# Kernel tuning notes

Measured on AMD Instinct MI355X. Metric: run time of the kernel, lower is better.

Reference implementation:

```python
import jax, jax.numpy as jnp
import numpy as np

TOP_K = 2


def setup_inputs() -> dict:
    key = jax.random.key(0)
    k1, k2 = jax.random.split(key)
    x = jax.random.normal(k1, (4, 4096, 2048), dtype=jnp.float32)
    W = jax.random.normal(k2, (64, 2048), dtype=jnp.float32) * (1.0 / np.sqrt(2048))
    return {"x": x, "W": W}


def reference(x, W):
    B, S, D = x.shape
    E = W.shape[0]
    # logits: [B*S, E] via linear router (no bias)
    flat = x.reshape(-1, D)
    logits = jnp.einsum('td,ed->te', flat, W)
    probs = jax.nn.softmax(logits, axis=-1)
    # eval path: top-k indices
    _, top_k_indices = jax.lax.top_k(probs, TOP_K)          # [T, K]
    # scatter 1s -> mask; scatter gathered probs -> router_probs (== probs*mask)
    router_mask = jax.nn.one_hot(top_k_indices, E, dtype=probs.dtype).sum(axis=-2)  # [T, E]
    router_probs = probs * router_mask
    # normalize (top_k > 1: gradient flows through the sum)
    router_probs = router_probs / router_probs.sum(axis=-1, keepdims=True)
    return (router_mask.reshape(B, S, E),
            top_k_indices.reshape(B, S, TOP_K),
            router_probs.reshape(B, S, E),
            probs.reshape(B, S, E))
```

## Files before the change

### kernel.cpp

```cpp
#include <hip/hip_runtime.h>
#include <math.h>


#define D_DIM 2048
#define E_DIM 64

typedef __bf16 bf16x8 __attribute__((ext_vector_type(8)));
typedef unsigned short us8 __attribute__((ext_vector_type(8)));
typedef float f32x4 __attribute__((ext_vector_type(4)));

static __device__ __forceinline__ unsigned short f2bf(float f) {
    unsigned int u = __float_as_uint(f);
    u += 0x7fffu + ((u >> 16) & 1u);
    return (unsigned short)(u >> 16);
}
static __device__ __forceinline__ float bf2f(unsigned short h) {
    return __uint_as_float(((unsigned int)h) << 16);
}
static __device__ __forceinline__ void split4(const float4 v, ushort4* h, ushort4* l) {
    h->x = f2bf(v.x); l->x = f2bf(v.x - bf2f(h->x));
    h->y = f2bf(v.y); l->y = f2bf(v.y - bf2f(h->y));
    h->z = f2bf(v.z); l->z = f2bf(v.z - bf2f(h->z));
    h->w = f2bf(v.w); l->w = f2bf(v.w - bf2f(h->w));
}

static __device__ __forceinline__ void gld_lds16(const void* g, void* l) {
    __builtin_amdgcn_global_load_lds(
        (const __attribute__((address_space(1))) unsigned int*)g,
        (__attribute__((address_space(3))) unsigned int*)l,
        16, 0, 0);
}

__global__ __launch_bounds__(256, 1) void convert_w(
    const float4* __restrict__ W4, unsigned short* __restrict__ WH,
    unsigned short* __restrict__ WL)
{
    int i = blockIdx.x * 256 + threadIdx.x;
    float4 v = W4[i];
    ushort4 h, l;
    split4(v, &h, &l);
    *(ushort4*)&WH[i * 4] = h;
    *(ushort4*)&WL[i * 4] = l;
}

template<int KS>
__global__ __launch_bounds__(256, 3) void gemm_part(
    const float* __restrict__ x,
    const unsigned short* __restrict__ WHg, const unsigned short* __restrict__ WLg,
    float* __restrict__ P, int T)
{
    __shared__ __align__(16) float XF[2][64 * 64];

    const int tid  = threadIdx.x;
    const int lane = tid & 63;
    const int wv   = tid >> 6;
    const int quad = lane >> 4;
    const int l16  = lane & 15;

    const int ntb = T >> 6;
    const int tb  = blockIdx.x % ntb;
    const int ksl = blockIdx.x / ntb;
    const int t0  = tb << 6;
    const int NCH = (D_DIM / KS) >> 6;
    const int k0  = ksl * (D_DIM / KS);

    f32x4 acc[4];
    #pragma unroll
    for (int n = 0; n < 4; ++n) { f32x4 z = {0.f, 0.f, 0.f, 0.f}; acc[n] = z; }

    const int srow = wv * 4 + (lane >> 4);
    const int scg  = lane & 15;

    #pragma unroll
    for (int i = 0; i < 4; ++i) {
        int row = i * 16 + srow;
        int cg  = scg ^ (row & 15);
        gld_lds16(x + (size_t)(t0 + row) * D_DIM + k0 + cg * 4,
                  &XF[0][(i * 256 + wv * 64) * 4]);
    }

    for (int ch = 0; ch < NCH; ++ch) {
        const int buf = ch & 1;
        const int kc  = k0 + (ch << 6);

        bf16x8 bh[2][4], bl[2][4];
        #pragma unroll
        for (int ks2 = 0; ks2 < 2; ++ks2)
            #pragma unroll
            for (int n = 0; n < 4; ++n) {
                const size_t wo = (size_t)(n * 16 + l16) * D_DIM + kc + ks2 * 32 + quad * 8;
                bh[ks2][n] = *(const bf16x8*)(WHg + wo);
                bl[ks2][n] = *(const bf16x8*)(WLg + wo);
            }

        {
            const int chn = (ch + 1) & (NCH - 1);
            const int kcn = k0 + (chn << 6);
            #pragma unroll
            for (int i = 0; i < 4; ++i) {
                int row = i * 16 + srow;
                int cg  = scg ^ (row & 15);
                gld_lds16(x + (size_t)(t0 + row) * D_DIM + kcn + cg * 4,
                          &XF[buf ^ 1][(i * 256 + wv * 64) * 4]);
            }
        }

        asm volatile("s_waitcnt vmcnt(20)" ::: "memory");
        __builtin_amdgcn_s_barrier();

        #pragma unroll
        for (int ks2 = 0; ks2 < 2; ++ks2) {
            const int tr = wv * 16 + l16;
            const int c0 = ks2 * 8 + quad * 2;
            float4 xa = *(const float4*)&XF[buf][(tr * 16 + ( c0      ^ (tr & 15))) * 4];
            float4 xb = *(const float4*)&XF[buf][(tr * 16 + ((c0 + 1) ^ (tr & 15))) * 4];
            ushort4 h0, l0, h1, l1;
            split4(xa, &h0, &l0);
            split4(xb, &h1, &l1);
            union { us8 u; bf16x8 b; } ua, ul;
            ua.u = (us8){h0.x, h0.y, h0.z, h0.w, h1.x, h1.y, h1.z, h1.w};
            ul.u = (us8){l0.x, l0.y, l0.z, l0.w, l1.x, l1.y, l1.z, l1.w};

            #pragma unroll
            for (int n = 0; n < 4; ++n) {
                acc[n] = __builtin_amdgcn_mfma_f32_16x16x32_bf16(ua.b, bh[ks2][n], acc[n], 0, 0, 0);
                acc[n] = __builtin_amdgcn_mfma_f32_16x16x32_bf16(ul.b, bh[ks2][n], acc[n], 0, 0, 0);
                acc[n] = __builtin_amdgcn_mfma_f32_16x16x32_bf16(ua.b, bl[ks2][n], acc[n], 0, 0, 0);
            }
        }

        __builtin_amdgcn_s_barrier();
    }

    float* Pb = P + ((size_t)ksl * T + t0) * 64;
    #pragma unroll
    for (int n = 0; n < 4; ++n)
        #pragma unroll
        for (int r = 0; r < 4; ++r)
            Pb[(wv * 16 + quad * 4 + r) * 64 + n * 16 + l16] = acc[n][r];
}

template<int KS>
__global__ __launch_bounds__(256, 4) void reduce_router(
    const float* __restrict__ P, int T,
    float* __restrict__ mask_out, float* __restrict__ idx_out,
    float* __restrict__ rp_out, float* __restrict__ probs_out)
{
    const int tid  = threadIdx.x;
    const int lane = tid & 63;
    const int wv   = tid >> 6;

    for (int i = 0; i < 4; ++i) {
        int t = blockIdx.x * 16 + wv * 4 + i;
        float v = 0.f;
        #pragma unroll
        for (int s = 0; s < KS; ++s)
            v += P[((size_t)s * T + t) * 64 + lane];

        float bv = v; int bi = lane;
        #pragma unroll
        for (int off = 1; off < 64; off <<= 1) {
            float ov = __shfl_xor(bv, off, 64);
            int   oi = __shfl_xor(bi, off, 64);
            bool take = (ov > bv) || (ov == bv && oi < bi);
            bv = take ? ov : bv;
            bi = take ? oi : bi;
        }
        float m = bv; int i1 = bi;

        float p = __expf(v - m);
        float s = p;
        #pragma unroll
        for (int off = 1; off < 64; off <<= 1) s += __shfl_xor(s, off, 64);
        float prob = p / s;

        float v2 = (lane == i1) ? -INFINITY : v;
        float bv2 = v2; int bi2 = lane;
        #pragma unroll
        for (int off = 1; off < 64; off <<= 1) {
            float ov = __shfl_xor(bv2, off, 64);
            int   oi = __shfl_xor(bi2, off, 64);
            bool take = (ov > bv2) || (ov == bv2 && oi < bi2);
            bv2 = take ? ov : bv2;
            bi2 = take ? oi : bi2;
        }
        int i2 = bi2;

        float pd = __shfl(prob, i1, 64) + __shfl(prob, i2, 64);
        bool top = (lane == i1) || (lane == i2);

        mask_out[(size_t)t * 64 + lane]  = top ? 1.f : 0.f;
        rp_out[(size_t)t * 64 + lane]    = top ? prob / pd : 0.f;
        probs_out[(size_t)t * 64 + lane] = prob;
        if (lane == 0) {
            idx_out[(size_t)t * 2]     = (float)i1;
            idx_out[(size_t)t * 2 + 1] = (float)i2;
        }
    }
}

extern "C" void kernel_launch(void* const* d_in, const int* in_sizes, int n_in,
                              void* d_out, int out_size, void* d_ws, size_t ws_size,
                              hipStream_t stream) {
    const float* x = (const float*)d_in[0];
    const float* W = (const float*)d_in[1];
    float* out = (float*)d_out;

    const int T  = in_sizes[0] / D_DIM;
    const int WN = in_sizes[1];

    unsigned short* WH = (unsigned short*)d_ws;
    unsigned short* WL = WH + WN;
    float* P = (float*)(WL + WN);

    float* mask_out  = out;
    float* idx_out   = out + (size_t)T * E_DIM;
    float* rp_out    = idx_out + (size_t)T * 2;
    float* probs_out = rp_out + (size_t)T * E_DIM;

    const size_t avail = ws_size - (size_t)WN * 4;
    const size_t slice_bytes = (size_t)T * 64 * 4;

    convert_w<<<dim3(WN / 1024), dim3(256), 0, stream>>>((const float4*)W, WH, WL);

    if (avail >= 4 * slice_bytes) {
        gemm_part<4><<<dim3((T / 64) * 4), dim3(256), 0, stream>>>(x, WH, WL, P, T);
        reduce_router<4><<<dim3(T / 16), dim3(256), 0, stream>>>(
            P, T, mask_out, idx_out, rp_out, probs_out);
    } else if (avail >= 2 * slice_bytes) {
        gemm_part<2><<<dim3((T / 64) * 2), dim3(256), 0, stream>>>(x, WH, WL, P, T);
        reduce_router<2><<<dim3(T / 16), dim3(256), 0, stream>>>(
            P, T, mask_out, idx_out, rp_out, probs_out);
    } else {
        gemm_part<1><<<dim3(T / 64), dim3(256), 0, stream>>>(x, WH, WL, P, T);
        reduce_router<1><<<dim3(T / 16), dim3(256), 0, stream>>>(
            P, T, mask_out, idx_out, rp_out, probs_out);
    }
}
```

Measured before the change: 229.0 us.

## Restructure router GEMM into single-wave blocks with 4-stage LDS ring and pre-swizzled W

Replaces the 256-thread, 64-token GEMM blocks with 64-thread single-wave blocks over 32 tokens. They use a 4-deep LDS ring of x tiles loaded asynchronously three steps ahead, with no block barriers. W is pre-packed into an MFMA-fragment-ordered hi/lo bf16 layout so each lane does one contiguous 16-byte load per fragment, and the next step's W fragments are register double-buffered. The split-K factor is fixed at 4 and the workspace-size fallbacks are dropped. This aims to hide memory latency with finer-grained waves and deeper prefetch, at the cost of more blocks and redundant W traffic per token.

```diff
diff --git a/kernel.cpp b/kernel.cpp
--- a/kernel.cpp
+++ b/kernel.cpp
@@ -4,10 +4,14 @@
 
 #define D_DIM 2048
 #define E_DIM 64
+#define KS 4
+#define KSTEPS 16
 
 typedef __bf16 bf16x8 __attribute__((ext_vector_type(8)));
 typedef unsigned short us8 __attribute__((ext_vector_type(8)));
 typedef float f32x4 __attribute__((ext_vector_type(4)));
+
+#define FENCE asm volatile("" ::: "memory")
 
 static __device__ __forceinline__ unsigned short f2bf(float f) {
     unsigned int u = __float_as_uint(f);
@@ -32,115 +36,126 @@
 }
 
 __global__ __launch_bounds__(256, 1) void convert_w(
-    const float4* __restrict__ W4, unsigned short* __restrict__ WH,
-    unsigned short* __restrict__ WL)
+    const float* __restrict__ W, unsigned short* __restrict__ WB)
 {
-    int i = blockIdx.x * 256 + threadIdx.x;
-    float4 v = W4[i];
-    ushort4 h, l;
-    split4(v, &h, &l);
-    *(ushort4*)&WH[i * 4] = h;
-    *(ushort4*)&WL[i * 4] = l;
-}
-
-template<int KS>
-__global__ __launch_bounds__(256, 3) void gemm_part(
-    const float* __restrict__ x,
-    const unsigned short* __restrict__ WHg, const unsigned short* __restrict__ WLg,
+    int u = blockIdx.x * 256 + threadIdx.x;
+    int lane = u & 63;
+    int r = u >> 6;
+    int h = r & 1;  r >>= 1;
+    int n = r & 3;  int sg = r >> 2;
+    int E  = n * 16 + (lane & 15);
+    int k0 = sg * 32 + (lane >> 4) * 8;
+    const float4* src = (const float4*)(W + (size_t)E * D_DIM + k0);
+    float4 a = src[0], b = src[1];
+    ushort4 ha, la, hb, lb;
+    split4(a, &ha, &la);
+    split4(b, &hb, &lb);
+    us8 out = h ? (us8){la.x, la.y, la.z, la.w, lb.x, lb.y, lb.z, lb.w}
+                : (us8){ha.x, ha.y, ha.z, ha.w, hb.x, hb.y, hb.z, hb.w};
+    *(us8*)(WB + (size_t)u * 8) = out;
+}
+
+__global__ __launch_bounds__(64, 2) void gemm_part(
+    const float* __restrict__ x, const unsigned short* __restrict__ WB,
     float* __restrict__ P, int T)
 {
-    __shared__ __align__(16) float XF[2][64 * 64];
-
-    const int tid  = threadIdx.x;
-    const int lane = tid & 63;
-    const int wv   = tid >> 6;
+    __shared__ __align__(16) float RING[4][1024];
+
+    const int lane = threadIdx.x;
     const int quad = lane >> 4;
     const int l16  = lane & 15;
 
-    const int ntb = T >> 6;
+    const int ntb = T >> 5;
     const int tb  = blockIdx.x % ntb;
     const int ksl = blockIdx.x / ntb;
-    const int t0  = tb << 6;
-    const int NCH = (D_DIM / KS) >> 6;
-    const int k0  = ksl * (D_DIM / KS);
-
-    f32x4 acc[4];
+    const int t0  = tb << 5;
+    const int kb  = ksl * (D_DIM / KS);
+
+    const int srow = lane >> 2;
+    const int scg  = (lane & 3) ^ ((lane >> 3) & 3);
+
+    f32x4 acc[2][4];
     #pragma unroll
-    for (int n = 0; n < 4; ++n) { f32x4 z = {0.f, 0.f, 0.f, 0.f}; acc[n] = z; }
-
-    const int srow = wv * 4 + (lane >> 4);
-    const int scg  = lane & 15;
+    for (int g = 0; g < 2; ++g)
+        #pragma unroll
+        for (int n = 0; n < 4; ++n) { f32x4 z = {0.f, 0.f, 0.f, 0.f}; acc[g][n] = z; }
+
+    auto stage = [&](int s) {
+        const int kc = kb + s * 32;
+        #pragma unroll
+        for (int j = 0; j < 4; ++j) {
+            int g = j >> 1, jj = j & 1;
+            int row = g * 16 + (srow & 3) + ((srow >> 2) << 2);
+            gld_lds16(x + (size_t)(t0 + row) * D_DIM + kc + jj * 16 + scg * 4,
+                      &RING[s & 3][j * 256]);
+        }
+    };
+
+    auto loadW = [&](int s, bf16x8 Wf[4][2]) {
+        const int sg = ksl * KSTEPS + s;
+        #pragma unroll
+        for (int n = 0; n < 4; ++n)
+            #pragma unroll
+            for (int h = 0; h < 2; ++h)
+                Wf[n][h] = *(const bf16x8*)(WB + ((((size_t)sg * 4 + n) * 2 + h) * 64 + lane) * 8);
+    };
+
+    bf16x8 Wc[4][2], Wn[4][2];
+    stage(0);  FENCE;
+    loadW(0, Wc); FENCE;
+    stage(1);  FENCE;
+    stage(2);  FENCE;
+
+    const float fsw = 0.f; (void)fsw;
 
     #pragma unroll
-    for (int i = 0; i < 4; ++i) {
-        int row = i * 16 + srow;
-        int cg  = scg ^ (row & 15);
-        gld_lds16(x + (size_t)(t0 + row) * D_DIM + k0 + cg * 4,
-                  &XF[0][(i * 256 + wv * 64) * 4]);
-    }
-
-    for (int ch = 0; ch < NCH; ++ch) {
-        const int buf = ch & 1;
-        const int kc  = k0 + (ch << 6);
-
-        bf16x8 bh[2][4], bl[2][4];
-        #pragma unroll
-        for (int ks2 = 0; ks2 < 2; ++ks2)
-            #pragma unroll
-            for (int n = 0; n < 4; ++n) {
-                const size_t wo = (size_t)(n * 16 + l16) * D_DIM + kc + ks2 * 32 + quad * 8;
-                bh[ks2][n] = *(const bf16x8*)(WHg + wo);
-                bl[ks2][n] = *(const bf16x8*)(WLg + wo);
-            }
-
-        {
-            const int chn = (ch + 1) & (NCH - 1);
-            const int kcn = k0 + (chn << 6);
-            #pragma unroll
-            for (int i = 0; i < 4; ++i) {
-                int row = i * 16 + srow;
-                int cg  = scg ^ (row & 15);
-                gld_lds16(x + (size_t)(t0 + row) * D_DIM + kcn + cg * 4,
-                          &XF[buf ^ 1][(i * 256 + wv * 64) * 4]);
-            }
-        }
-
-        asm volatile("s_waitcnt vmcnt(20)" ::: "memory");
-        __builtin_amdgcn_s_barrier();
-
-        #pragma unroll
-        for (int ks2 = 0; ks2 < 2; ++ks2) {
-            const int tr = wv * 16 + l16;
-            const int c0 = ks2 * 8 + quad * 2;
-            float4 xa = *(const float4*)&XF[buf][(tr * 16 + ( c0      ^ (tr & 15))) * 4];
-            float4 xb = *(const float4*)&XF[buf][(tr * 16 + ((c0 + 1) ^ (tr & 15))) * 4];
+    for (int s = 0; s < KSTEPS; ++s) {
+        if (s + 1 < KSTEPS) loadW(s + 1, Wn);
+        if (s + 3 < KSTEPS) stage(s + 3);
+
+        if (s < 2)            asm volatile("s_waitcnt vmcnt(28)" ::: "memory");
+        else if (s < KSTEPS - 3) asm volatile("s_waitcnt vmcnt(36)" ::: "memory");
+        else                  asm volatile("s_waitcnt vmcnt(16)" ::: "memory");
+
+        const int f = (l16 >> 1) & 3;
+        const int jj = quad >> 1;
+        const int c  = (2 * quad) & 3;
+        #pragma unroll
+        for (int g = 0; g < 2; ++g) {
+            const float* B = &RING[s & 3][g * 512 + jj * 256];
+            float4 xa = *(const float4*)&B[(l16 * 4 + ( c      ^ f)) * 4];
+            float4 xb = *(const float4*)&B[(l16 * 4 + ((c + 1) ^ f)) * 4];
             ushort4 h0, l0, h1, l1;
             split4(xa, &h0, &l0);
             split4(xb, &h1, &l1);
             union { us8 u; bf16x8 b; } ua, ul;
             ua.u = (us8){h0.x, h0.y, h0.z, h0.w, h1.x, h1.y, h1.z, h1.w};
             ul.u = (us8){l0.x, l0.y, l0.z, l0.w, l1.x, l1.y, l1.z, l1.w};
-
             #pragma unroll
             for (int n = 0; n < 4; ++n) {
-                acc[n] = __builtin_amdgcn_mfma_f32_16x16x32_bf16(ua.b, bh[ks2][n], acc[n], 0, 0, 0);
-                acc[n] = __builtin_amdgcn_mfma_f32_16x16x32_bf16(ul.b, bh[ks2][n], acc[n], 0, 0, 0);
-                acc[n] = __builtin_amdgcn_mfma_f32_16x16x32_bf16(ua.b, bl[ks2][n], acc[n], 0, 0, 0);
+                acc[g][n] = __builtin_amdgcn_mfma_f32_16x16x32_bf16(ua.b, Wc[n][0], acc[g][n], 0, 0, 0);
+                acc[g][n] = __builtin_amdgcn_mfma_f32_16x16x32_bf16(ul.b, Wc[n][0], acc[g][n], 0, 0, 0);
+                acc[g][n] = __builtin_amdgcn_mfma_f32_16x16x32_bf16(ua.b, Wc[n][1], acc[g][n], 0, 0, 0);
             }
         }
 
-        __builtin_amdgcn_s_barrier();
+        #pragma unroll
+        for (int n = 0; n < 4; ++n)
+            #pragma unroll
+            for (int h = 0; h < 2; ++h)
+                Wc[n][h] = Wn[n][h];
     }
 
     float* Pb = P + ((size_t)ksl * T + t0) * 64;
     #pragma unroll
-    for (int n = 0; n < 4; ++n)
-        #pragma unroll
-        for (int r = 0; r < 4; ++r)
-            Pb[(wv * 16 + quad * 4 + r) * 64 + n * 16 + l16] = acc[n][r];
-}
-
-template<int KS>
+    for (int g = 0; g < 2; ++g)
+        #pragma unroll
+        for (int n = 0; n < 4; ++n)
+            #pragma unroll
+            for (int r = 0; r < 4; ++r)
+                Pb[(g * 16 + quad * 4 + r) * 64 + n * 16 + l16] = acc[g][n][r];
+}
+
 __global__ __launch_bounds__(256, 4) void reduce_router(
     const float* __restrict__ P, int T,
     float* __restrict__ mask_out, float* __restrict__ idx_out,
@@ -209,31 +224,16 @@
     const int T  = in_sizes[0] / D_DIM;
     const int WN = in_sizes[1];
 
-    unsigned short* WH = (unsigned short*)d_ws;
-    unsigned short* WL = WH + WN;
-    float* P = (float*)(WL + WN);
+    unsigned short* WB = (unsigned short*)d_ws;
+    float* P = (float*)(WB + (size_t)WN * 2);
 
     float* mask_out  = out;
     float* idx_out   = out + (size_t)T * E_DIM;
     float* rp_out    = idx_out + (size_t)T * 2;
     float* probs_out = rp_out + (size_t)T * E_DIM;
 
-    const size_t avail = ws_size - (size_t)WN * 4;
-    const size_t slice_bytes = (size_t)T * 64 * 4;
-
-    convert_w<<<dim3(WN / 1024), dim3(256), 0, stream>>>((const float4*)W, WH, WL);
-
-    if (avail >= 4 * slice_bytes) {
-        gemm_part<4><<<dim3((T / 64) * 4), dim3(256), 0, stream>>>(x, WH, WL, P, T);
-        reduce_router<4><<<dim3(T / 16), dim3(256), 0, stream>>>(
-            P, T, mask_out, idx_out, rp_out, probs_out);
-    } else if (avail >= 2 * slice_bytes) {
-        gemm_part<2><<<dim3((T / 64) * 2), dim3(256), 0, stream>>>(x, WH, WL, P, T);
-        reduce_router<2><<<dim3(T / 16), dim3(256), 0, stream>>>(
-            P, T, mask_out, idx_out, rp_out, probs_out);
-    } else {
-        gemm_part<1><<<dim3(T / 64), dim3(256), 0, stream>>>(x, WH, WL, P, T);
-        reduce_router<1><<<dim3(T / 16), dim3(256), 0, stream>>>(
-            P, T, mask_out, idx_out, rp_out, probs_out);
-    }
-}
+    convert_w<<<dim3((WN * 2) / 8 / 256), dim3(256), 0, stream>>>(W, WB);
+    gemm_part<<<dim3((T / 32) * KS), dim3(64), 0, stream>>>(x, WB, P, T);
+    reduce_router<<<dim3(T / 16), dim3(256), 0, stream>>>(
+        P, T, mask_out, idx_out, rp_out, probs_out);
+}
```

After: 210.0 us. 1.09x faster.
